# Kernel tuning notes

Hardware: AMD Instinct MI355X
Metric: run time of the kernel (lower is better)

## Reference

```python
import jax, jax.numpy as jnp
import numpy as np

IN_FEATURES = 1024
ACT_BITS = 4


def _hadamard(size: int) -> np.ndarray:
    # Sylvester construction, normalized: H(n) = Sylvester(n) / sqrt(n)
    h = np.array([[1.0]], dtype=np.float64)
    while h.shape[0] < size:
        h = np.block([[h, h], [h, -h]])
    return (h / np.sqrt(size)).astype(np.float32)


def _quantize_activations(x, bits=ACT_BITS):
    pos = 2 ** (bits - 1) - 1  # 7
    neg = 2 ** (bits - 1)      # 8
    scale = jnp.clip(jnp.max(jnp.abs(jax.lax.stop_gradient(x)), axis=-1, keepdims=True), 1e-5) / pos
    q = jnp.clip(jnp.round(x / scale), -neg, pos) * scale
    return x + jax.lax.stop_gradient(q - x)  # STE


def _ternary_quantize_ste(w):
    scale = jnp.clip(jnp.mean(jnp.abs(jax.lax.stop_gradient(w)), axis=1, keepdims=True), 1e-5)
    n = w / scale
    tern = jnp.where(n > 0.5, 1.0, jnp.where(n < -0.5, -1.0, 0.0))
    q = tern * scale
    return w + jax.lax.stop_gradient(q - w)  # STE


def setup_inputs() -> dict:
    key = jax.random.key(0)
    k1, k2 = jax.random.split(key)
    x = jax.random.normal(k1, (8, 8192, IN_FEATURES), dtype=jnp.float32)
    # master weight ~ kaiming-uniform-ish scale
    bound = 1.0 / np.sqrt(IN_FEATURES)
    weight = jax.random.uniform(k2, (1024, IN_FEATURES), dtype=jnp.float32, minval=-bound, maxval=bound)
    return {"x": x, "weight": weight}


def reference(x, weight):
    H = jnp.asarray(_hadamard(IN_FEATURES))  # [in, in]
    xh = x @ H                                # Hadamard precondition on input
    xq = _quantize_activations(xh)            # per-token 4-bit symmetric quant (STE)
    wq = _ternary_quantize_ste(weight)        # per-row ternary quant (STE)
    return jnp.einsum('bsi,oi->bso', xq, wq)  # F.linear, no bias
```

## Files before the change

### kernel.cpp

```cpp
#include <hip/hip_runtime.h>
#include <stdint.h>

typedef int v4i __attribute__((ext_vector_type(4)));
typedef float float4_t __attribute__((ext_vector_type(4)));

#define K_DIM 1024
#define N_DIM 1024
#define BM 128
#define BN 128

__device__ __forceinline__ void gload16(const void* g, void* l) {
  __builtin_amdgcn_global_load_lds(
      (const __attribute__((address_space(1))) unsigned int*)g,
      (__attribute__((address_space(3))) unsigned int*)l, 16, 0, 0);
}

#define MFMA_I8 __builtin_amdgcn_mfma_i32_16x16x64_i8

#define BAR_LDS()                                             \
  do {                                                        \
    asm volatile("s_waitcnt lgkmcnt(0)" ::: "memory");        \
    __builtin_amdgcn_s_barrier();                             \
  } while (0)

__global__ __launch_bounds__(256) void fwht_quant_kernel(
    const float* __restrict__ x, int8_t* __restrict__ qx,
    float* __restrict__ ascale, int M) {
  const int lane = threadIdx.x & 63;
  const int wid = threadIdx.x >> 6;
  const long token = (long)blockIdx.x * 4 + wid;
  if (token >= M) return;
  const float4_t* xr4 = (const float4_t*)(x + token * K_DIM);

  float v[16];
#pragma unroll
  for (int i = 0; i < 4; ++i) {
    float4_t f = xr4[lane * 4 + i];
#pragma unroll
    for (int c = 0; c < 4; ++c) v[i * 4 + c] = f[c];
  }
#pragma unroll
  for (int s = 1; s <= 8; s <<= 1) {
#pragma unroll
    for (int r = 0; r < 16; ++r)
      if ((r & s) == 0) {
        float a0 = v[r], b0 = v[r | s];
        v[r] = a0 + b0;
        v[r | s] = a0 - b0;
      }
  }
#pragma unroll
  for (int m = 1; m <= 32; m <<= 1) {
    const float sg = (lane & m) ? -1.0f : 1.0f;
#pragma unroll
    for (int r = 0; r < 16; ++r) {
      float p = __shfl_xor(v[r], m, 64);
      v[r] = fmaf(sg, v[r], p);
    }
  }
  float mx = 0.f;
#pragma unroll
  for (int r = 0; r < 16; ++r) mx = fmaxf(mx, fabsf(v[r]));
#pragma unroll
  for (int m = 32; m >= 1; m >>= 1) mx = fmaxf(mx, __shfl_xor(mx, m, 64));
  const float scale = fmaxf(mx * 0.03125f, 1e-5f) * (1.0f / 7.0f);
  if (lane == 0) ascale[token] = scale;
  const float inv = 0.03125f / scale;

  v4i pk;
#pragma unroll
  for (int i = 0; i < 4; ++i) {
    int packed = 0;
#pragma unroll
    for (int c = 0; c < 4; ++c) {
      float q = rintf(v[i * 4 + c] * inv);
      q = fminf(7.f, fmaxf(-8.f, q));
      packed |= ((int)q & 0xff) << (8 * c);
    }
    pk[i] = packed;
  }
  *(v4i*)(qx + token * K_DIM + lane * 16) = pk;
}

__global__ __launch_bounds__(256) void wquant_kernel(
    const float* __restrict__ w, int8_t* __restrict__ qw,
    float* __restrict__ wscale) {
  const int lane = threadIdx.x & 63;
  const int wid = threadIdx.x >> 6;
  const int row = blockIdx.x * 4 + wid;
  const float* wr = w + (long)row * K_DIM;

  float v[16];
  float s = 0.f;
  const float4_t* wr4 = (const float4_t*)wr;
#pragma unroll
  for (int rr = 0; rr < 4; ++rr) {
    float4_t f = wr4[rr * 64 + lane];
#pragma unroll
    for (int c = 0; c < 4; ++c) {
      v[rr * 4 + c] = f[c];
      s += fabsf(f[c]);
    }
  }
#pragma unroll
  for (int m = 32; m >= 1; m >>= 1) s += __shfl_xor(s, m, 64);
  const float scale = fmaxf(s * (1.0f / 1024.0f), 1e-5f);
  if (lane == 0) wscale[row] = scale;

  int8_t* qr = qw + (long)row * K_DIM;
#pragma unroll
  for (int rr = 0; rr < 4; ++rr) {
    int packed = 0;
#pragma unroll
    for (int c = 0; c < 4; ++c) {
      float n = v[rr * 4 + c] / scale;
      int tv = (n > 0.5f) ? 1 : ((n < -0.5f) ? -1 : 0);
      packed |= (tv & 0xff) << (8 * c);
    }
    *(int*)(qr + rr * 256 + lane * 4) = packed;
  }
}

__global__ __launch_bounds__(256) void gemm_i8_kernel(
    const int8_t* __restrict__ A, const int8_t* __restrict__ B,
    const float* __restrict__ asc, const float* __restrict__ wsc,
    float* __restrict__ C, int M) {
  __shared__ __align__(16) int8_t smem[2][32768];
  float* tr = (float*)smem;

  const int t = threadIdx.x;
  const int lane = t & 63;
  const int wm = (t >> 6) >> 1;
  const int wn = (t >> 6) & 1;
  const int rl = lane & 15;
  const int kb = lane >> 4;

  const int swz = ((int)blockIdx.x & 7) * 512 + ((int)blockIdx.x >> 3);
  const long bm = swz >> 3;
  const int bn = swz & 7;

  const int chunkoff = (((t & 7) ^ ((t >> 3) & 7)) << 4);
  const int8_t* gA = A + (bm * BM + (t >> 3)) * (long)K_DIM + chunkoff;
  const int8_t* gB = B + ((long)bn * BN + (t >> 3)) * K_DIM + chunkoff;

  const int sw0 = ((kb ^ (rl & 7)) << 4);
  const int sw1 = (((4 + kb) ^ (rl & 7)) << 4);
  const int arow = (wm * 64 + rl) * 128;
  const int brow = (wn * 64 + rl) * 128;

  v4i acc[4][4] = {};

#define STAGE(p, ks)                                         \
  gload16(gA + (ks), smem[p] + t * 16);                      \
  gload16(gA + (ks) + 32 * K_DIM, smem[p] + 4096 + t * 16);  \
  gload16(gA + (ks) + 64 * K_DIM, smem[p] + 8192 + t * 16);  \
  gload16(gA + (ks) + 96 * K_DIM, smem[p] + 12288 + t * 16); \
  gload16(gB + (ks), smem[p] + 16384 + t * 16);              \
  gload16(gB + (ks) + 32 * K_DIM, smem[p] + 20480 + t * 16); \
  gload16(gB + (ks) + 64 * K_DIM, smem[p] + 24576 + t * 16); \
  gload16(gB + (ks) + 96 * K_DIM, smem[p] + 28672 + t * 16);

  STAGE(0, 0);
  __syncthreads();

#pragma unroll
  for (int kt = 0; kt < 8; ++kt) {
    const int p = kt & 1;
    if (kt < 7) {
      STAGE(p ^ 1, (kt + 1) * 128);
    }
    const int8_t* Al = smem[p];
    const int8_t* Bl = smem[p] + 16384;
#pragma unroll
    for (int ks2 = 0; ks2 < 2; ++ks2) {
      const int sw = ks2 ? sw1 : sw0;
      v4i a[4], b[4];
#pragma unroll
      for (int i = 0; i < 4; ++i)
        a[i] = *(const v4i*)(Al + arow + i * 2048 + sw);
#pragma unroll
      for (int j = 0; j < 4; ++j)
        b[j] = *(const v4i*)(Bl + brow + j * 2048 + sw);
#pragma unroll
      for (int i = 0; i < 4; ++i)
#pragma unroll
        for (int j = 0; j < 4; ++j)
          acc[i][j] = MFMA_I8(a[i], b[j], acc[i][j], 0, 0, 0);
    }
    __syncthreads();
  }
#undef STAGE

  const long rowg0 = bm * BM + wm * 64;
  const int colg0 = bn * BN + wn * 64;
#pragma unroll
  for (int c = 0; c < 2; ++c) {
    if (wm == c) {
#pragma unroll
      for (int i = 0; i < 4; ++i) {
        float as[4];
#pragma unroll
        for (int r = 0; r < 4; ++r) as[r] = asc[rowg0 + i * 16 + kb * 4 + r];
#pragma unroll
        for (int j = 0; j < 4; ++j) {
          const float ws = wsc[colg0 + j * 16 + rl];
#pragma unroll
          for (int r = 0; r < 4; ++r)
            tr[(i * 16 + kb * 4 + r) * 132 + wn * 64 + j * 16 + rl] =
                (float)acc[i][j][r] * as[r] * ws;
        }
      }
    }
    BAR_LDS();
#pragma unroll
    for (int it = 0; it < 8; ++it) {
      const int idx = t + it * 256;
      const int rl2 = idx >> 5;
      const int c4 = (idx & 31) * 4;
      const float4_t val = *(const float4_t*)(tr + rl2 * 132 + c4);
      __builtin_nontemporal_store(
          val, (float4_t*)(C + (bm * BM + c * 64 + rl2) * (long)N_DIM + bn * BN + c4));
    }
    if (c == 0) BAR_LDS();
  }
}

extern "C" void kernel_launch(void* const* d_in, const int* in_sizes, int n_in,
                              void* d_out, int out_size, void* d_ws, size_t ws_size,
                              hipStream_t stream) {
  const float* x = (const float*)d_in[0];
  const float* w = (const float*)d_in[1];
  float* out = (float*)d_out;
  const int M = in_sizes[0] / K_DIM;

  int8_t* qx = (int8_t*)d_ws;
  int8_t* qw = qx + (size_t)M * K_DIM;
  float* ascale = (float*)(qw + (size_t)N_DIM * K_DIM);
  float* wscale = ascale + M;

  fwht_quant_kernel<<<(M + 3) / 4, 256, 0, stream>>>(x, qx, ascale, M);
  wquant_kernel<<<N_DIM / 4, 256, 0, stream>>>(w, qw, wscale);
  gemm_i8_kernel<<<(M / BM) * (N_DIM / BN), 256, 0, stream>>>(qx, qw, ascale, wscale, out, M);
}
```

Before: 167.4 us.

## Pack quantized activations as offset 4-bit nibbles and unpack in GEMM

Activations are stored as unsigned 4-bit values (offset by 8), two per byte, which halves the intermediate activation buffer written by the FWHT kernel and read by the GEMM. The GEMM unpacks the nibbles into int8 lanes after loading from LDS, and the weight kernel now records per-row ternary sums so the epilogue can subtract the 8*sum offset. This cuts global traffic for A and its LDS footprint, at the cost of extra ALU work for unpacking and a new swizzle layout for A tiles.

```diff
diff --git a/kernel.cpp b/kernel.cpp
--- a/kernel.cpp
+++ b/kernel.cpp
@@ -2,6 +2,7 @@
 #include <stdint.h>
 
 typedef int v4i __attribute__((ext_vector_type(4)));
+typedef int v2i __attribute__((ext_vector_type(2)));
 typedef float float4_t __attribute__((ext_vector_type(4)));
 
 #define K_DIM 1024
@@ -24,7 +25,7 @@
   } while (0)
 
 __global__ __launch_bounds__(256) void fwht_quant_kernel(
-    const float* __restrict__ x, int8_t* __restrict__ qx,
+    const float* __restrict__ x, int8_t* __restrict__ qxp,
     float* __restrict__ ascale, int M) {
   const int lane = threadIdx.x & 63;
   const int wid = threadIdx.x >> 6;
@@ -67,24 +68,28 @@
   if (lane == 0) ascale[token] = scale;
   const float inv = 0.03125f / scale;
 
-  v4i pk;
-#pragma unroll
-  for (int i = 0; i < 4; ++i) {
-    int packed = 0;
-#pragma unroll
-    for (int c = 0; c < 4; ++c) {
-      float q = rintf(v[i * 4 + c] * inv);
-      q = fminf(7.f, fmaxf(-8.f, q));
-      packed |= ((int)q & 0xff) << (8 * c);
-    }
-    pk[i] = packed;
-  }
-  *(v4i*)(qx + token * K_DIM + lane * 16) = pk;
+  int u[16];
+#pragma unroll
+  for (int r = 0; r < 16; ++r) {
+    float q = rintf(v[r] * inv);
+    q = fminf(7.f, fmaxf(-8.f, q));
+    u[r] = (int)q + 8;
+  }
+  v2i pk;
+  int dw0 = 0, dw1 = 0;
+#pragma unroll
+  for (int j = 0; j < 4; ++j) {
+    dw0 |= ((u[j] | (u[j + 8] << 4)) & 0xff) << (8 * j);
+    dw1 |= ((u[j + 4] | (u[j + 12] << 4)) & 0xff) << (8 * j);
+  }
+  pk[0] = dw0;
+  pk[1] = dw1;
+  *(v2i*)(qxp + token * 512 + lane * 8) = pk;
 }
 
 __global__ __launch_bounds__(256) void wquant_kernel(
     const float* __restrict__ w, int8_t* __restrict__ qw,
-    float* __restrict__ wscale) {
+    float* __restrict__ wscale, int* __restrict__ tsum) {
   const int lane = threadIdx.x & 63;
   const int wid = threadIdx.x >> 6;
   const int row = blockIdx.x * 4 + wid;
@@ -108,6 +113,7 @@
   if (lane == 0) wscale[row] = scale;
 
   int8_t* qr = qw + (long)row * K_DIM;
+  int tloc = 0;
 #pragma unroll
   for (int rr = 0; rr < 4; ++rr) {
     int packed = 0;
@@ -115,17 +121,21 @@
     for (int c = 0; c < 4; ++c) {
       float n = v[rr * 4 + c] / scale;
       int tv = (n > 0.5f) ? 1 : ((n < -0.5f) ? -1 : 0);
+      tloc += tv;
       packed |= (tv & 0xff) << (8 * c);
     }
     *(int*)(qr + rr * 256 + lane * 4) = packed;
   }
+#pragma unroll
+  for (int m = 32; m >= 1; m >>= 1) tloc += __shfl_xor(tloc, m, 64);
+  if (lane == 0) tsum[row] = tloc;
 }
 
 __global__ __launch_bounds__(256) void gemm_i8_kernel(
-    const int8_t* __restrict__ A, const int8_t* __restrict__ B,
+    const int8_t* __restrict__ Aq, const int8_t* __restrict__ B,
     const float* __restrict__ asc, const float* __restrict__ wsc,
-    float* __restrict__ C, int M) {
-  __shared__ __align__(16) int8_t smem[2][32768];
+    const int* __restrict__ tsum, float* __restrict__ C, int M) {
+  __shared__ __align__(16) int8_t smem[49152];
   float* tr = (float*)smem;
 
   const int t = threadIdx.x;
@@ -139,26 +149,32 @@
   const long bm = swz >> 3;
   const int bn = swz & 7;
 
+  const int arowS = t >> 2;
+  const int apsS = (t & 3) ^ ((arowS >> 1) & 3);
+  const int8_t* gA = Aq + (bm * BM + arowS) * 512L + apsS * 16;
   const int chunkoff = (((t & 7) ^ ((t >> 3) & 7)) << 4);
-  const int8_t* gA = A + (bm * BM + (t >> 3)) * (long)K_DIM + chunkoff;
   const int8_t* gB = B + ((long)bn * BN + (t >> 3)) * K_DIM + chunkoff;
 
+  const int fA = (rl >> 1) & 3;
+  const int aBase = (wm * 64 + rl) * 64 + (kb & 1) * 8;
+  const int psA0 = ((kb >> 1) ^ fA) * 16;
+  const int psA1 = ((2 + (kb >> 1)) ^ fA) * 16;
   const int sw0 = ((kb ^ (rl & 7)) << 4);
   const int sw1 = (((4 + kb) ^ (rl & 7)) << 4);
-  const int arow = (wm * 64 + rl) * 128;
   const int brow = (wn * 64 + rl) * 128;
 
   v4i acc[4][4] = {};
 
-#define STAGE(p, ks)                                         \
-  gload16(gA + (ks), smem[p] + t * 16);                      \
-  gload16(gA + (ks) + 32 * K_DIM, smem[p] + 4096 + t * 16);  \
-  gload16(gA + (ks) + 64 * K_DIM, smem[p] + 8192 + t * 16);  \
-  gload16(gA + (ks) + 96 * K_DIM, smem[p] + 12288 + t * 16); \
-  gload16(gB + (ks), smem[p] + 16384 + t * 16);              \
-  gload16(gB + (ks) + 32 * K_DIM, smem[p] + 20480 + t * 16); \
-  gload16(gB + (ks) + 64 * K_DIM, smem[p] + 24576 + t * 16); \
-  gload16(gB + (ks) + 96 * K_DIM, smem[p] + 28672 + t * 16);
+#define STAGE(p, kt_)                                                   \
+  gload16(gA + (kt_) * 64, smem + (p)*8192 + t * 16);                   \
+  gload16(gA + 64 * 512 + (kt_) * 64, smem + (p)*8192 + 4096 + t * 16); \
+  gload16(gB + (kt_) * 128, smem + 16384 + (p)*16384 + t * 16);         \
+  gload16(gB + (kt_) * 128 + 32 * K_DIM,                                \
+          smem + 16384 + (p)*16384 + 4096 + t * 16);                    \
+  gload16(gB + (kt_) * 128 + 64 * K_DIM,                                \
+          smem + 16384 + (p)*16384 + 8192 + t * 16);                    \
+  gload16(gB + (kt_) * 128 + 96 * K_DIM,                                \
+          smem + 16384 + (p)*16384 + 12288 + t * 16);
 
   STAGE(0, 0);
   __syncthreads();
@@ -167,17 +183,24 @@
   for (int kt = 0; kt < 8; ++kt) {
     const int p = kt & 1;
     if (kt < 7) {
-      STAGE(p ^ 1, (kt + 1) * 128);
-    }
-    const int8_t* Al = smem[p];
-    const int8_t* Bl = smem[p] + 16384;
+      STAGE(p ^ 1, kt + 1);
+    }
+    const int8_t* Al = smem + p * 8192;
+    const int8_t* Bl = smem + 16384 + p * 16384;
 #pragma unroll
     for (int ks2 = 0; ks2 < 2; ++ks2) {
+      const int psA = ks2 ? psA1 : psA0;
       const int sw = ks2 ? sw1 : sw0;
       v4i a[4], b[4];
 #pragma unroll
-      for (int i = 0; i < 4; ++i)
-        a[i] = *(const v4i*)(Al + arow + i * 2048 + sw);
+      for (int i = 0; i < 4; ++i) {
+        v2i d = *(const v2i*)(Al + aBase + i * 1024 + psA);
+        const unsigned u0 = (unsigned)d[0], u1 = (unsigned)d[1];
+        a[i][0] = (int)(u0 & 0x0F0F0F0Fu);
+        a[i][1] = (int)(u1 & 0x0F0F0F0Fu);
+        a[i][2] = (int)((u0 >> 4) & 0x0F0F0F0Fu);
+        a[i][3] = (int)((u1 >> 4) & 0x0F0F0F0Fu);
+      }
 #pragma unroll
       for (int j = 0; j < 4; ++j)
         b[j] = *(const v4i*)(Bl + brow + j * 2048 + sw);
@@ -203,11 +226,13 @@
         for (int r = 0; r < 4; ++r) as[r] = asc[rowg0 + i * 16 + kb * 4 + r];
 #pragma unroll
         for (int j = 0; j < 4; ++j) {
-          const float ws = wsc[colg0 + j * 16 + rl];
+          const int col = colg0 + j * 16 + rl;
+          const float ws = wsc[col];
+          const int corr = tsum[col] << 3;
 #pragma unroll
           for (int r = 0; r < 4; ++r)
             tr[(i * 16 + kb * 4 + r) * 132 + wn * 64 + j * 16 + rl] =
-                (float)acc[i][j][r] * as[r] * ws;
+                (float)(acc[i][j][r] - corr) * as[r] * ws;
         }
       }
     }
@@ -233,12 +258,13 @@
   float* out = (float*)d_out;
   const int M = in_sizes[0] / K_DIM;
 
-  int8_t* qx = (int8_t*)d_ws;
-  int8_t* qw = qx + (size_t)M * K_DIM;
+  int8_t* qxp = (int8_t*)d_ws;
+  int8_t* qw = qxp + (size_t)M * 512;
   float* ascale = (float*)(qw + (size_t)N_DIM * K_DIM);
   float* wscale = ascale + M;
-
-  fwht_quant_kernel<<<(M + 3) / 4, 256, 0, stream>>>(x, qx, ascale, M);
-  wquant_kernel<<<N_DIM / 4, 256, 0, stream>>>(w, qw, wscale);
-  gemm_i8_kernel<<<(M / BM) * (N_DIM / BN), 256, 0, stream>>>(qx, qw, ascale, wscale, out, M);
-}
+  int* tsum = (int*)(wscale + N_DIM);
+
+  fwht_quant_kernel<<<(M + 3) / 4, 256, 0, stream>>>(x, qxp, ascale, M);
+  wquant_kernel<<<N_DIM / 4, 256, 0, stream>>>(w, qw, wscale, tsum);
+  gemm_i8_kernel<<<(M / BM) * (N_DIM / BN), 256, 0, stream>>>(qxp, qw, ascale, wscale, tsum, out, M);
+}
```

New measurement: 164.4 us. About the same (-1.8%).
